# Kernel tuning notes

Hardware: AMD Instinct MI355X
Metric: run time of the kernel (lower is better)

Reference implementation:

```python
import jax, jax.numpy as jnp
import numpy as np

B, H, N, C, E, D, L_OUT, LAYERS = 16, 64, 512, 3, 128, 32, 12, 2


def setup_inputs() -> dict:
    key = jax.random.key(0)
    ks = jax.random.split(key, 16)
    nrm = lambda k, s, sc=1.0: jax.random.normal(k, s, jnp.float32) * sc
    adj = jax.random.uniform(ks[0], (N, N), jnp.float32)
    adj = adj / adj.sum(axis=-1, keepdims=True)  # row-normalized prior adjacency
    return {
        "x_input": nrm(ks[1], (B, H, N, C)),
        "adj": adj,
        "Wf": nrm(ks[2], (3, E, 3 * C), 0.1),
        "Uf": nrm(ks[3], (3, E, E), 0.05),
        "bf": jnp.zeros((3, E), jnp.float32),
        "E1f": nrm(ks[4], (N, D)),
        "E2f": nrm(ks[5], (N, D)),
        "Wb": nrm(ks[6], (3, E, 3 * C), 0.1),
        "Ub": nrm(ks[7], (3, E, E), 0.05),
        "bb": jnp.zeros((3, E), jnp.float32),
        "E1b": nrm(ks[8], (N, D)),
        "E2b": nrm(ks[9], (N, D)),
        "dec_w": nrm(ks[10], (L_OUT, LAYERS, 2 * E), 0.05),  # Conv2d(layer_num->out_len, k=(1,2E)) squeezed
        "dec_b": jnp.zeros((L_OUT,), jnp.float32),
        "out_w": nrm(ks[11], (L_OUT, L_OUT), 0.1),  # 1x1 Conv2d squeezed
        "out_b": jnp.zeros((L_OUT,), jnp.float32),
    }


def _cell_step(c, xt, adj, A_dyn, W, U, b):
    # Graph-coupled GRU cell (IBNCell): xt [B,C,N], c [B,E,N].
    msg = jnp.concatenate(
        [xt,
         jnp.einsum('bcn,nm->bcm', xt, adj),      # prior-graph message passing
         jnp.einsum('bcn,nm->bcm', xt, A_dyn)],   # learned dynamic-graph message passing
        axis=1)  # [B, 3C, N]
    gx = jnp.einsum('goc,bcn->gbon', W, msg)  # 3 stacked gate projections
    r = jax.nn.sigmoid(gx[0] + jnp.einsum('oe,ben->bon', U[0], c) + b[0][:, None])
    u = jax.nn.sigmoid(gx[1] + jnp.einsum('oe,ben->bon', U[1], c) + b[1][:, None])
    g = jnp.tanh(gx[2] + jnp.einsum('oe,ben->bon', U[2], r * c) + b[2][:, None])
    return u * c + (1.0 - u) * g


def _forward(x_input, adj, Wf, Uf, bf, E1f, E2f, Wb, Ub, bb, E1b, E2b, dec_w, dec_b, out_w, out_b):
    # torch: x_input.transpose(-3,-1).transpose(-2,-1) -> [B,C,H,N]; scan layout [H,B,C,N]
    xs = jnp.transpose(x_input, (1, 0, 3, 2))
    A_f = jax.nn.softmax(jax.nn.relu(E1f @ E2f.T), axis=-1)  # dynamic adjacency, fwd cell
    A_b = jax.nn.softmax(jax.nn.relu(E1b @ E2b.T), axis=-1)  # dynamic adjacency, back cell
    c0 = jnp.zeros((xs.shape[1], Wf.shape[1], xs.shape[3]), xs.dtype)  # [B,E,N]

    def step_f(c, xt):
        cn = _cell_step(c, xt, adj, A_f, Wf, Uf, bf)
        return cn, None

    # Output only depends on the last timestep of the bidirectional concat:
    # forward branch -> final state after H steps; backward branch (after flip)
    # at t=H-1 -> its FIRST step (input x[H-1]). Dead per-step outputs elided.
    h_fwd, _ = jax.lax.scan(step_f, c0, xs)
    h_back0 = _cell_step(c0, xs[-1], adj, A_b, Wb, Ub, bb)
    last_ht = jnp.concatenate([h_fwd, h_back0], axis=1)  # [B, 2E, N]

    lt = jnp.transpose(last_ht, (0, 2, 1))  # [B, N, 2E]
    # layer loop z>0 is a no-op on current_layer_output -> final_result repeats last_ht
    final = jnp.broadcast_to(lt[:, None], (lt.shape[0], LAYERS, lt.shape[1], lt.shape[2]))
    h = jnp.einsum('blne,ole->bon', final, dec_w) + dec_b[:, None]  # decoder conv (1,2E)
    return jnp.einsum('oi,bin->bon', out_w, h) + out_b[:, None]  # 1x1 output conv -> [B,L_OUT,N]


def reference(x_input, adj, Wf, Uf, bf, E1f, E2f, Wb, Ub, bb, E1b, E2b, dec_w, dec_b, out_w, out_b):
    return _forward(x_input, adj, Wf, Uf, bf, E1f, E2f, Wb, Ub, bb, E1b, E2b, dec_w, dec_b, out_w, out_b)
```

## Files before the change

kernel.cpp:

```cpp
#include <hip/hip_runtime.h>


typedef _Float16 half8_t __attribute__((ext_vector_type(8)));
typedef float float4_t __attribute__((ext_vector_type(4)));

#define PIN(x) asm volatile("" : "+v"(x))

__device__ __forceinline__ float sigmoidf_(float x) {
  return __builtin_amdgcn_rcpf(1.f + __expf(-x));
}
__device__ __forceinline__ float tanhf_(float x) {
  return fmaf(-2.f, __builtin_amdgcn_rcpf(__expf(2.f * x) + 1.f), 1.f);
}

__global__ __launch_bounds__(256) void prep_kernel(
    const float* __restrict__ E1f, const float* __restrict__ E2f,
    const float* __restrict__ E1b, const float* __restrict__ E2b,
    const float* __restrict__ adj, const float* __restrict__ x,
    const float* __restrict__ Wf, const float* __restrict__ Uf,
    const float* __restrict__ bf, const float* __restrict__ Wb,
    const float* __restrict__ bb, _Float16* __restrict__ adjT,
    _Float16* __restrict__ AfT, _Float16* __restrict__ AbT,
    _Float16* __restrict__ xT16, _Float16* __restrict__ ufrag,
    _Float16* __restrict__ wbfrag) {
  int bid = blockIdx.x;
  int tid = threadIdx.x;
  if (bid >= 1288) {
    int bid2 = bid - 1288;
    int b = bid2 >> 6, t = bid2 & 63;
    const float2* xp = (const float2*)(x + (size_t)(b * 64 + t) * 1536);
    float2 f0 = xp[tid * 3], f1 = xp[tid * 3 + 1], f2 = xp[tid * 3 + 2];
    _Float16* dst = xT16 + (size_t)(b * 64 + t) * 1536;
    int n0_ = tid * 2;
    dst[n0_] = (_Float16)f0.x;
    dst[512 + n0_] = (_Float16)f0.y;
    dst[1024 + n0_] = (_Float16)f1.x;
    dst[n0_ + 1] = (_Float16)f1.y;
    dst[512 + n0_ + 1] = (_Float16)f2.x;
    dst[1024 + n0_ + 1] = (_Float16)f2.y;
    return;
  }
  if (bid >= 1272) {
    int r2 = bid - 1272;
    int gi = 1 + (r2 & 1);
    int og = r2 >> 1;
    for (int e = tid; e < 512; e += 256) {
      int lane = e >> 3, j = e & 7;
      int o = og * 16 + (lane & 15);
      int q = (lane >> 4) * 8 + j;
      float v = (q < 9) ? Wb[gi * 1152 + o * 9 + q]
                        : (q == 9 ? bb[gi * 128 + o] : 0.f);
      wbfrag[r2 * 512 + e] = (_Float16)v;
    }
    return;
  }
  if (bid >= 1152) {
    int r = bid - 1152;
    int kb = r % 5;
    int gi = (r / 5) % 3;
    int og = r / 15;
    for (int e = tid; e < 512; e += 256) {
      int lane = e >> 3, j = e & 7;
      int o = og * 16 + (lane & 15);
      int q4 = lane >> 4;
      float v;
      if (kb < 4) {
        v = Uf[gi * 16384 + o * 128 + kb * 32 + q4 * 8 + j];
      } else {
        int q = q4 * 8 + j;
        v = (q < 9) ? Wf[gi * 1152 + o * 9 + q]
                    : (q == 9 ? bf[gi * 128 + o] : 0.f);
      }
      ufrag[r * 512 + e] = (_Float16)v;
    }
    return;
  }
  if (bid >= 1024) {
    int base = (bid - 1024) * 4;
    for (int r = 0; r < 4; ++r) {
      int row = base + r;
      float v0 = adj[row * 512 + tid];
      float v1 = adj[row * 512 + tid + 256];
      adjT[(size_t)tid * 512 + row] = (_Float16)v0;
      adjT[(size_t)(tid + 256) * 512 + row] = (_Float16)v1;
    }
    return;
  }
  int which = bid >> 9;
  int row = bid & 511;
  const float* E1 = which ? E1b : E1f;
  const float* E2 = which ? E2b : E2f;
  _Float16* A = which ? AbT : AfT;
  __shared__ float e1s[32];
  __shared__ float red[256];
  if (tid < 32) e1s[tid] = E1[row * 32 + tid];
  __syncthreads();
  float s[2];
#pragma unroll
  for (int h = 0; h < 2; ++h) {
    int m = tid + h * 256;
    const float4* e2 = (const float4*)(E2 + m * 32);
    float acc = 0.f;
#pragma unroll
    for (int d4 = 0; d4 < 8; ++d4) {
      float4 v = e2[d4];
      acc = fmaf(v.x, e1s[d4 * 4 + 0], acc);
      acc = fmaf(v.y, e1s[d4 * 4 + 1], acc);
      acc = fmaf(v.z, e1s[d4 * 4 + 2], acc);
      acc = fmaf(v.w, e1s[d4 * 4 + 3], acc);
    }
    s[h] = fmaxf(acc, 0.f);
  }
  red[tid] = fmaxf(s[0], s[1]);
  __syncthreads();
  for (int off = 128; off > 0; off >>= 1) {
    if (tid < off) red[tid] = fmaxf(red[tid], red[tid + off]);
    __syncthreads();
  }
  float mx = red[0];
  __syncthreads();
  float e0 = __expf(s[0] - mx), e1v = __expf(s[1] - mx);
  red[tid] = e0 + e1v;
  __syncthreads();
  for (int off = 128; off > 0; off >>= 1) {
    if (tid < off) red[tid] += red[tid + off];
    __syncthreads();
  }
  float inv = __builtin_amdgcn_rcpf(red[0]);
  A[(size_t)tid * 512 + row] = (_Float16)(e0 * inv);
  A[(size_t)(tid + 256) * 512 + row] = (_Float16)(e1v * inv);
}

__global__ __launch_bounds__(256, 4) void msg_kernel(
    const _Float16* __restrict__ xT16, const _Float16* __restrict__ adjT,
    const _Float16* __restrict__ AfT, const _Float16* __restrict__ AbT,
    _Float16* __restrict__ msg16, _Float16* __restrict__ msgb16) {
  __shared__ __align__(8) _Float16 Sst[512 * 12];
  int tid = threadIdx.x;
  int t = blockIdx.x >> 4;
  int n0g = (blockIdx.x & 15) * 32;
  int lane = tid & 63, og = tid >> 6;
  int l15 = lane & 15, q4 = lane >> 4, q0 = q4 * 8;
  int nt = og & 1, mat = og >> 1;
  bool is63 = (t == 63);
  bool doAb = is63 && (mat == 0);

  const _Float16* Bmat = mat ? AfT : adjT;
  int n = n0g + nt * 16 + l15;

  const float4_t zero4 = {0.f, 0.f, 0.f, 0.f};
  float4_t acc[3], accb[3];
#pragma unroll
  for (int mt = 0; mt < 3; ++mt) { acc[mt] = zero4; accb[mt] = zero4; }

  for (int kb = 0; kb < 16; ++kb) {
    half8_t b0 = *(const half8_t*)&Bmat[(size_t)n * 512 + kb * 32 + q0];
    half8_t b2;
    if (doAb) b2 = *(const half8_t*)&AbT[(size_t)n * 512 + kb * 32 + q0];
#pragma unroll
    for (int mt = 0; mt < 3; ++mt) {
      int m = mt * 16 + l15;
      int bm = (m * 21846) >> 16;
      int cm = m - bm * 3;
      half8_t a = *(const half8_t*)
          &xT16[((size_t)(bm * 64 + t) * 3 + cm) * 512 + kb * 32 + q0];
      acc[mt] = __builtin_amdgcn_mfma_f32_16x16x32_f16(a, b0, acc[mt], 0, 0, 0);
      if (doAb)
        accb[mt] = __builtin_amdgcn_mfma_f32_16x16x32_f16(a, b2, accb[mt], 0, 0, 0);
    }
  }

  for (int i = tid; i < 512; i += 256) {
    int tb = i >> 5, nl = i & 31;
    int nn = n0g + nl;
    _Float16* row = &Sst[i * 12];
#pragma unroll
    for (int c = 0; c < 3; ++c)
      row[c] = xT16[((size_t)(tb * 64 + t) * 3 + c) * 512 + nn];
    row[9] = (_Float16)1.f;
    row[10] = (_Float16)0.f;
    row[11] = (_Float16)0.f;
  }
#pragma unroll
  for (int mt = 0; mt < 3; ++mt)
#pragma unroll
    for (int r = 0; r < 4; ++r) {
      int m = mt * 16 + q4 * 4 + r;
      int tb = (m * 21846) >> 16;
      int c = m - tb * 3;
      Sst[((size_t)tb * 32 + nt * 16 + l15) * 12 + 3 + mat * 3 + c] =
          (_Float16)acc[mt][r];
    }
  __syncthreads();
  for (int i = tid; i < 512; i += 256) {
    int tb = i >> 5, nl = i & 31;
    const uint2* s = (const uint2*)&Sst[i * 12];
    uint2* dst = (uint2*)&msg16[((size_t)(t * 16 + tb) * 512 + n0g + nl) * 12];
    dst[0] = s[0]; dst[1] = s[1]; dst[2] = s[2];
  }
  if (is63) {
    __syncthreads();
    if (mat == 0) {
#pragma unroll
      for (int mt = 0; mt < 3; ++mt)
#pragma unroll
        for (int r = 0; r < 4; ++r) {
          int m = mt * 16 + q4 * 4 + r;
          int tb = (m * 21846) >> 16;
          int c = m - tb * 3;
          Sst[((size_t)tb * 32 + nt * 16 + l15) * 12 + 6 + c] = (_Float16)accb[mt][r];
        }
    }
    __syncthreads();
    for (int i = tid; i < 512; i += 256) {
      int tb = i >> 5, nl = i & 31;
      const uint2* s = (const uint2*)&Sst[i * 12];
      uint2* dst = (uint2*)&msgb16[((size_t)tb * 512 + n0g + nl) * 12];
      dst[0] = s[0]; dst[1] = s[1]; dst[2] = s[2];
    }
  }
}

__global__ __launch_bounds__(512, 4) void rec_kernel(
    const _Float16* __restrict__ msg16, const _Float16* __restrict__ msgb16,
    const _Float16* __restrict__ ufrag, const _Float16* __restrict__ wbfrag,
    const float* __restrict__ dec_w, const float* __restrict__ dec_b,
    const float* __restrict__ out_w, const float* __restrict__ out_b,
    float* __restrict__ out) {
  __shared__ __align__(16) _Float16 Cbuf[4 * 64 * 8];
  __shared__ __align__(16) _Float16 Gbuf[4 * 64 * 8];
  __shared__ float hf_lds[128 * 16];
  __shared__ float hb_lds[128 * 16];
  __shared__ float hdec_lds[12 * 16];
  int tid = threadIdx.x, bid = blockIdx.x;
  int b = bid >> 5;
  int n0 = (bid & 31) * 16;
  int lane = tid & 63, og = tid >> 6;
  int l15 = lane & 15, q4 = lane >> 4;

  half8_t afrag[3][5];
#pragma unroll
  for (int gi = 0; gi < 3; ++gi)
#pragma unroll
    for (int kb = 0; kb < 5; ++kb) {
      afrag[gi][kb] = *(const half8_t*)
          &ufrag[(size_t)(((og * 3 + gi) * 5 + kb) * 512) + lane * 8];
      PIN(afrag[gi][kb]);
    }

  if (tid < 256) {
    uint4 z; z.x = z.y = z.z = z.w = 0;
    ((uint4*)Cbuf)[tid] = z;
  }
  float cr[4] = {0.f, 0.f, 0.f, 0.f};
  __syncthreads();

  const float4_t zero4 = {0.f, 0.f, 0.f, 0.f};
  union H4U { _Float16 h[4]; unsigned long long u; };
  union U16 { uint4 u4; half8_t h8; };
  unsigned odd = q4 & 1;
  const char* mrow = (const char*)msg16 + ((size_t)(b * 512 + n0 + l15)) * 24;
  const size_t tstride = (size_t)16 * 512 * 24;

  U16 bu;
  {
    uint4 lo = *(const uint4*)mrow;
    uint2 hi = *(const uint2*)(mrow + 16);
    bu.u4.x = odd ? hi.x : lo.x;
    bu.u4.y = odd ? hi.y : lo.y;
    bu.u4.z = odd ? 0u : lo.z;
    bu.u4.w = odd ? 0u : lo.w;
  }
  half8_t bm_cur = bu.h8;

  int kb_w = og >> 1;
  int lane_w = ((og & 1) * 2 + (q4 >> 1)) * 16 + l15;
  int j0 = (q4 & 1) * 4;

  for (int t = 0; t < 64; ++t) {
    int tn = (t < 63) ? t + 1 : 63;
    const char* p = mrow + (size_t)tn * tstride;
    uint4 lo = *(const uint4*)p;
    uint2 hi = *(const uint2*)(p + 16);

    half8_t cf[4];
#pragma unroll
    for (int kb = 0; kb < 4; ++kb)
      cf[kb] = *(const half8_t*)&Cbuf[(kb * 64 + lane) * 8];

    float4_t accr = zero4, accu = zero4;
#pragma unroll
    for (int kb = 0; kb < 4; ++kb) {
      accr = __builtin_amdgcn_mfma_f32_16x16x32_f16(afrag[0][kb], cf[kb], accr, 0, 0, 0);
      accu = __builtin_amdgcn_mfma_f32_16x16x32_f16(afrag[1][kb], cf[kb], accu, 0, 0, 0);
    }
    accr = __builtin_amdgcn_mfma_f32_16x16x32_f16(afrag[0][4], bm_cur, accr, 0, 0, 0);
    accu = __builtin_amdgcn_mfma_f32_16x16x32_f16(afrag[1][4], bm_cur, accu, 0, 0, 0);
    float4_t accg = __builtin_amdgcn_mfma_f32_16x16x32_f16(afrag[2][4], bm_cur, zero4, 0, 0, 0);

    {
      H4U v;
#pragma unroll
      for (int r = 0; r < 4; ++r)
        v.h[r] = (_Float16)(sigmoidf_(accr[r]) * cr[r]);
      *(unsigned long long*)&Gbuf[(kb_w * 64 + lane_w) * 8 + j0] = v.u;
    }
    __syncthreads();

    half8_t gf[4];
#pragma unroll
    for (int kb = 0; kb < 4; ++kb)
      gf[kb] = *(const half8_t*)&Gbuf[(kb * 64 + lane) * 8];
#pragma unroll
    for (int kb = 0; kb < 4; ++kb)
      accg = __builtin_amdgcn_mfma_f32_16x16x32_f16(afrag[2][kb], gf[kb], accg, 0, 0, 0);

    {
      H4U v;
#pragma unroll
      for (int r = 0; r < 4; ++r) {
        float uu = sigmoidf_(accu[r]);
        float gg = tanhf_(accg[r]);
        float cn = fmaf(uu, cr[r] - gg, gg);
        cr[r] = cn;
        v.h[r] = (_Float16)cn;
      }
      *(unsigned long long*)&Cbuf[(kb_w * 64 + lane_w) * 8 + j0] = v.u;
    }
    __syncthreads();

    bu.u4.x = odd ? hi.x : lo.x;
    bu.u4.y = odd ? hi.y : lo.y;
    bu.u4.z = odd ? 0u : lo.z;
    bu.u4.w = odd ? 0u : lo.w;
    bm_cur = bu.h8;
  }

  {
    const char* p = (const char*)msgb16 + ((size_t)(b * 512 + n0 + l15)) * 24;
    uint4 lo = *(const uint4*)p;
    uint2 hi = *(const uint2*)(p + 16);
    U16 bb2;
    bb2.u4.x = odd ? hi.x : lo.x;
    bb2.u4.y = odd ? hi.y : lo.y;
    bb2.u4.z = odd ? 0u : lo.z;
    bb2.u4.w = odd ? 0u : lo.w;
    half8_t au_f = *(const half8_t*)&wbfrag[(size_t)((og * 2 + 0) * 512) + lane * 8];
    half8_t ag_f = *(const half8_t*)&wbfrag[(size_t)((og * 2 + 1) * 512) + lane * 8];
    float4_t au = __builtin_amdgcn_mfma_f32_16x16x32_f16(au_f, bb2.h8, zero4, 0, 0, 0);
    float4_t ag = __builtin_amdgcn_mfma_f32_16x16x32_f16(ag_f, bb2.h8, zero4, 0, 0, 0);
#pragma unroll
    for (int r = 0; r < 4; ++r) {
      int row = og * 16 + q4 * 4 + r;
      float uu = sigmoidf_(au[r]);
      float gg = tanhf_(ag[r]);
      hb_lds[row * 16 + l15] = (1.f - uu) * gg;
      hf_lds[row * 16 + l15] = cr[r];
    }
  }
  __syncthreads();

  if (tid < 192) {
    int i = tid >> 4, cc = tid & 15;
    const float* dwa = dec_w + (size_t)i * 512;
    const float* dwb = dwa + 256;
    float hd = dec_b[i];
    for (int e = 0; e < 128; ++e) {
      hd = fmaf(dwa[e] + dwb[e], hf_lds[e * 16 + cc], hd);
      hd = fmaf(dwa[128 + e] + dwb[128 + e], hb_lds[e * 16 + cc], hd);
    }
    hdec_lds[i * 16 + cc] = hd;
  }
  __syncthreads();
  if (tid < 192) {
    int o = tid >> 4, cc = tid & 15;
    float v = out_b[o];
#pragma unroll
    for (int i = 0; i < 12; ++i) v = fmaf(out_w[o * 12 + i], hdec_lds[i * 16 + cc], v);
    out[((size_t)(b * 12 + o)) * 512 + n0 + cc] = v;
  }
}

extern "C" void kernel_launch(void* const* d_in, const int* in_sizes, int n_in,
                              void* d_out, int out_size, void* d_ws, size_t ws_size,
                              hipStream_t stream) {
  (void)in_sizes; (void)n_in; (void)out_size; (void)ws_size;
  const float* x     = (const float*)d_in[0];
  const float* adj   = (const float*)d_in[1];
  const float* Wf    = (const float*)d_in[2];
  const float* Uf    = (const float*)d_in[3];
  const float* bf    = (const float*)d_in[4];
  const float* E1f   = (const float*)d_in[5];
  const float* E2f   = (const float*)d_in[6];
  const float* Wb    = (const float*)d_in[7];
  const float* bb    = (const float*)d_in[9];
  const float* E1b   = (const float*)d_in[10];
  const float* E2b   = (const float*)d_in[11];
  const float* dec_w = (const float*)d_in[12];
  const float* dec_b = (const float*)d_in[13];
  const float* out_w = (const float*)d_in[14];
  const float* out_b = (const float*)d_in[15];

  _Float16* h      = (_Float16*)d_ws;
  _Float16* adjT   = h;
  _Float16* AfT    = h + 262144;
  _Float16* AbT    = h + 524288;
  _Float16* xT16   = h + 786432;
  _Float16* ufrag  = h + 2359296;
  _Float16* wbfrag = h + 2420736;
  _Float16* msg16  = h + 2428928;
  _Float16* msgb16 = h + 8720384;

  prep_kernel<<<2312, 256, 0, stream>>>(E1f, E2f, E1b, E2b, adj, x, Wf, Uf, bf,
                                        Wb, bb, adjT, AfT, AbT, xT16, ufrag, wbfrag);
  msg_kernel<<<1024, 256, 0, stream>>>(xT16, adjT, AfT, AbT, msg16, msgb16);
  rec_kernel<<<512, 512, 0, stream>>>(msg16, msgb16, ufrag, wbfrag,
                                      dec_w, dec_b, out_w, out_b, (float*)d_out);
}
```

Measured before the change: 220.0 us.

## Fold exp2 scaling into gate weights and tile-transpose adjacency matrices

Gate weight fragments are pre-scaled by -log2(e) or 2*log2(e) so the recurrent loop's sigmoid and tanh become a raw exp2 plus a reciprocal, with no per-element multiply. Half conversion now uses packed round-toward-zero converts. The strided transposed writes of adj and the softmax matrices in prep are replaced by row-major writes plus a separate LDS-tiled transpose kernel, aiming for coalesced global stores. This costs an extra kernel launch and a second pass over the softmax matrices, and the fp16 rounding of the scaled weights changes slightly.

```diff
diff --git a/kernel.cpp b/kernel.cpp
--- a/kernel.cpp
+++ b/kernel.cpp
@@ -2,31 +2,27 @@
 
 
 typedef _Float16 half8_t __attribute__((ext_vector_type(8)));
+typedef __fp16 fp16x2_t __attribute__((ext_vector_type(2)));
 typedef float float4_t __attribute__((ext_vector_type(4)));
 
 #define PIN(x) asm volatile("" : "+v"(x))
 
-__device__ __forceinline__ float sigmoidf_(float x) {
-  return __builtin_amdgcn_rcpf(1.f + __expf(-x));
-}
-__device__ __forceinline__ float tanhf_(float x) {
-  return fmaf(-2.f, __builtin_amdgcn_rcpf(__expf(2.f * x) + 1.f), 1.f);
-}
+__device__ __forceinline__ float exp2_(float x) { return __builtin_amdgcn_exp2f(x); }
+__device__ __forceinline__ float rcp_(float x) { return __builtin_amdgcn_rcpf(x); }
 
 __global__ __launch_bounds__(256) void prep_kernel(
     const float* __restrict__ E1f, const float* __restrict__ E2f,
     const float* __restrict__ E1b, const float* __restrict__ E2b,
-    const float* __restrict__ adj, const float* __restrict__ x,
-    const float* __restrict__ Wf, const float* __restrict__ Uf,
-    const float* __restrict__ bf, const float* __restrict__ Wb,
-    const float* __restrict__ bb, _Float16* __restrict__ adjT,
-    _Float16* __restrict__ AfT, _Float16* __restrict__ AbT,
+    const float* __restrict__ x, const float* __restrict__ Wf,
+    const float* __restrict__ Uf, const float* __restrict__ bf,
+    const float* __restrict__ Wb, const float* __restrict__ bb,
+    _Float16* __restrict__ AfR, _Float16* __restrict__ AbR,
     _Float16* __restrict__ xT16, _Float16* __restrict__ ufrag,
     _Float16* __restrict__ wbfrag) {
   int bid = blockIdx.x;
   int tid = threadIdx.x;
-  if (bid >= 1288) {
-    int bid2 = bid - 1288;
+  if (bid >= 1160) {
+    int bid2 = bid - 1160;
     int b = bid2 >> 6, t = bid2 & 63;
     const float2* xp = (const float2*)(x + (size_t)(b * 64 + t) * 1536);
     float2 f0 = xp[tid * 3], f1 = xp[tid * 3 + 1], f2 = xp[tid * 3 + 2];
@@ -40,25 +36,27 @@
     dst[1024 + n0_ + 1] = (_Float16)f2.y;
     return;
   }
-  if (bid >= 1272) {
-    int r2 = bid - 1272;
+  if (bid >= 1144) {
+    int r2 = bid - 1144;
     int gi = 1 + (r2 & 1);
     int og = r2 >> 1;
+    float scl = (gi == 2) ? 2.8853902f : -1.4426950f;
     for (int e = tid; e < 512; e += 256) {
       int lane = e >> 3, j = e & 7;
       int o = og * 16 + (lane & 15);
       int q = (lane >> 4) * 8 + j;
       float v = (q < 9) ? Wb[gi * 1152 + o * 9 + q]
                         : (q == 9 ? bb[gi * 128 + o] : 0.f);
-      wbfrag[r2 * 512 + e] = (_Float16)v;
+      wbfrag[r2 * 512 + e] = (_Float16)(v * scl);
     }
     return;
   }
-  if (bid >= 1152) {
-    int r = bid - 1152;
+  if (bid >= 1024) {
+    int r = bid - 1024;
     int kb = r % 5;
     int gi = (r / 5) % 3;
     int og = r / 15;
+    float scl = (gi == 2) ? 2.8853902f : -1.4426950f;
     for (int e = tid; e < 512; e += 256) {
       int lane = e >> 3, j = e & 7;
       int o = og * 16 + (lane & 15);
@@ -71,18 +69,7 @@
         v = (q < 9) ? Wf[gi * 1152 + o * 9 + q]
                     : (q == 9 ? bf[gi * 128 + o] : 0.f);
       }
-      ufrag[r * 512 + e] = (_Float16)v;
-    }
-    return;
-  }
-  if (bid >= 1024) {
-    int base = (bid - 1024) * 4;
-    for (int r = 0; r < 4; ++r) {
-      int row = base + r;
-      float v0 = adj[row * 512 + tid];
-      float v1 = adj[row * 512 + tid + 256];
-      adjT[(size_t)tid * 512 + row] = (_Float16)v0;
-      adjT[(size_t)(tid + 256) * 512 + row] = (_Float16)v1;
+      ufrag[r * 512 + e] = (_Float16)(v * scl);
     }
     return;
   }
@@ -90,7 +77,7 @@
   int row = bid & 511;
   const float* E1 = which ? E1b : E1f;
   const float* E2 = which ? E2b : E2f;
-  _Float16* A = which ? AbT : AfT;
+  _Float16* A = which ? AbR : AfR;
   __shared__ float e1s[32];
   __shared__ float red[256];
   if (tid < 32) e1s[tid] = E1[row * 32 + tid];
@@ -126,9 +113,37 @@
     if (tid < off) red[tid] += red[tid + off];
     __syncthreads();
   }
-  float inv = __builtin_amdgcn_rcpf(red[0]);
-  A[(size_t)tid * 512 + row] = (_Float16)(e0 * inv);
-  A[(size_t)(tid + 256) * 512 + row] = (_Float16)(e1v * inv);
+  float inv = rcp_(red[0]);
+  A[(size_t)row * 512 + tid] = (_Float16)(e0 * inv);
+  A[(size_t)row * 512 + tid + 256] = (_Float16)(e1v * inv);
+}
+
+__global__ __launch_bounds__(256) void transpose_kernel(
+    const float* __restrict__ adj, const _Float16* __restrict__ AfR,
+    const _Float16* __restrict__ AbR, _Float16* __restrict__ adjT,
+    _Float16* __restrict__ AfT, _Float16* __restrict__ AbT) {
+  __shared__ _Float16 T[64][65];
+  int bid = blockIdx.x;
+  int mat = bid >> 6;
+  int tile = bid & 63;
+  int tr = tile >> 3, tc = tile & 7;
+  int t = threadIdx.x;
+  int r = t >> 2, cb = (t & 3) * 16;
+  if (mat == 0) {
+    const float* s = adj + (size_t)(tr * 64 + r) * 512 + tc * 64 + cb;
+#pragma unroll
+    for (int i = 0; i < 16; ++i) T[r][cb + i] = (_Float16)s[i];
+  } else {
+    const _Float16* s =
+        (mat == 1 ? AfR : AbR) + (size_t)(tr * 64 + r) * 512 + tc * 64 + cb;
+#pragma unroll
+    for (int i = 0; i < 16; ++i) T[r][cb + i] = s[i];
+  }
+  __syncthreads();
+  _Float16* d = (mat == 0 ? adjT : mat == 1 ? AfT : AbT) +
+                (size_t)(tc * 64 + r) * 512 + tr * 64 + cb;
+#pragma unroll
+  for (int i = 0; i < 16; ++i) d[i] = T[cb + i][r];
 }
 
 __global__ __launch_bounds__(256, 4) void msg_kernel(
@@ -227,14 +242,15 @@
     const float* __restrict__ dec_w, const float* __restrict__ dec_b,
     const float* __restrict__ out_w, const float* __restrict__ out_b,
     float* __restrict__ out) {
-  __shared__ __align__(16) _Float16 Cbuf[4 * 64 * 8];
-  __shared__ __align__(16) _Float16 Gbuf[4 * 64 * 8];
+  __shared__ __align__(16) _Float16 Cbuf[2048];
+  __shared__ __align__(16) _Float16 Gbuf[2048];
   __shared__ float hf_lds[128 * 16];
   __shared__ float hb_lds[128 * 16];
   __shared__ float hdec_lds[12 * 16];
   int tid = threadIdx.x, bid = blockIdx.x;
   int b = bid >> 5;
-  int n0 = (bid & 31) * 16;
+  int nt = bid & 31;
+  int n0 = nt * 16;
   int lane = tid & 63, og = tid >> 6;
   int l15 = lane & 15, q4 = lane >> 4;
 
@@ -253,14 +269,13 @@
     ((uint4*)Cbuf)[tid] = z;
   }
   float cr[4] = {0.f, 0.f, 0.f, 0.f};
-  __syncthreads();
 
   const float4_t zero4 = {0.f, 0.f, 0.f, 0.f};
-  union H4U { _Float16 h[4]; unsigned long long u; };
+  union H4U { fp16x2_t h2[2]; unsigned long long u; };
   union U16 { uint4 u4; half8_t h8; };
   unsigned odd = q4 & 1;
+  const size_t tstride = (size_t)16 * 512 * 24;
   const char* mrow = (const char*)msg16 + ((size_t)(b * 512 + n0 + l15)) * 24;
-  const size_t tstride = (size_t)16 * 512 * 24;
 
   U16 bu;
   {
@@ -271,11 +286,12 @@
     bu.u4.z = odd ? 0u : lo.z;
     bu.u4.w = odd ? 0u : lo.w;
   }
-  half8_t bm_cur = bu.h8;
+  half8_t bm = bu.h8;
 
   int kb_w = og >> 1;
   int lane_w = ((og & 1) * 2 + (q4 >> 1)) * 16 + l15;
   int j0 = (q4 & 1) * 4;
+  __syncthreads();
 
   for (int t = 0; t < 64; ++t) {
     int tn = (t < 63) ? t + 1 : 63;
@@ -294,37 +310,42 @@
       accr = __builtin_amdgcn_mfma_f32_16x16x32_f16(afrag[0][kb], cf[kb], accr, 0, 0, 0);
       accu = __builtin_amdgcn_mfma_f32_16x16x32_f16(afrag[1][kb], cf[kb], accu, 0, 0, 0);
     }
-    accr = __builtin_amdgcn_mfma_f32_16x16x32_f16(afrag[0][4], bm_cur, accr, 0, 0, 0);
-    accu = __builtin_amdgcn_mfma_f32_16x16x32_f16(afrag[1][4], bm_cur, accu, 0, 0, 0);
-    float4_t accg = __builtin_amdgcn_mfma_f32_16x16x32_f16(afrag[2][4], bm_cur, zero4, 0, 0, 0);
+    accr = __builtin_amdgcn_mfma_f32_16x16x32_f16(afrag[0][4], bm, accr, 0, 0, 0);
+    accu = __builtin_amdgcn_mfma_f32_16x16x32_f16(afrag[1][4], bm, accu, 0, 0, 0);
+    float4_t accg = __builtin_amdgcn_mfma_f32_16x16x32_f16(afrag[2][4], bm, zero4, 0, 0, 0);
+
+    {
+      float rc0 = rcp_(1.f + exp2_(accr[0])) * cr[0];
+      float rc1 = rcp_(1.f + exp2_(accr[1])) * cr[1];
+      float rc2 = rcp_(1.f + exp2_(accr[2])) * cr[2];
+      float rc3 = rcp_(1.f + exp2_(accr[3])) * cr[3];
+      H4U v;
+      v.h2[0] = __builtin_amdgcn_cvt_pkrtz(rc0, rc1);
+      v.h2[1] = __builtin_amdgcn_cvt_pkrtz(rc2, rc3);
+      *(unsigned long long*)&Gbuf[(kb_w * 64 + lane_w) * 8 + j0] = v.u;
+    }
+    __syncthreads();
+
+    half8_t gf[4];
+#pragma unroll
+    for (int kb = 0; kb < 4; ++kb)
+      gf[kb] = *(const half8_t*)&Gbuf[(kb * 64 + lane) * 8];
+#pragma unroll
+    for (int kb = 0; kb < 4; ++kb)
+      accg = __builtin_amdgcn_mfma_f32_16x16x32_f16(afrag[2][kb], gf[kb], accg, 0, 0, 0);
 
     {
       H4U v;
-#pragma unroll
-      for (int r = 0; r < 4; ++r)
-        v.h[r] = (_Float16)(sigmoidf_(accr[r]) * cr[r]);
-      *(unsigned long long*)&Gbuf[(kb_w * 64 + lane_w) * 8 + j0] = v.u;
-    }
-    __syncthreads();
-
-    half8_t gf[4];
-#pragma unroll
-    for (int kb = 0; kb < 4; ++kb)
-      gf[kb] = *(const half8_t*)&Gbuf[(kb * 64 + lane) * 8];
-#pragma unroll
-    for (int kb = 0; kb < 4; ++kb)
-      accg = __builtin_amdgcn_mfma_f32_16x16x32_f16(afrag[2][kb], gf[kb], accg, 0, 0, 0);
-
-    {
-      H4U v;
+      float cn[4];
 #pragma unroll
       for (int r = 0; r < 4; ++r) {
-        float uu = sigmoidf_(accu[r]);
-        float gg = tanhf_(accg[r]);
-        float cn = fmaf(uu, cr[r] - gg, gg);
-        cr[r] = cn;
-        v.h[r] = (_Float16)cn;
+        float uu = rcp_(1.f + exp2_(accu[r]));
+        float gg = fmaf(-2.f, rcp_(exp2_(accg[r]) + 1.f), 1.f);
+        cn[r] = fmaf(uu, cr[r] - gg, gg);
+        cr[r] = cn[r];
       }
+      v.h2[0] = __builtin_amdgcn_cvt_pkrtz(cn[0], cn[1]);
+      v.h2[1] = __builtin_amdgcn_cvt_pkrtz(cn[2], cn[3]);
       *(unsigned long long*)&Cbuf[(kb_w * 64 + lane_w) * 8 + j0] = v.u;
     }
     __syncthreads();
@@ -333,7 +354,7 @@
     bu.u4.y = odd ? hi.y : lo.y;
     bu.u4.z = odd ? 0u : lo.z;
     bu.u4.w = odd ? 0u : lo.w;
-    bm_cur = bu.h8;
+    bm = bu.h8;
   }
 
   {
@@ -352,8 +373,8 @@
 #pragma unroll
     for (int r = 0; r < 4; ++r) {
       int row = og * 16 + q4 * 4 + r;
-      float uu = sigmoidf_(au[r]);
-      float gg = tanhf_(ag[r]);
+      float uu = rcp_(1.f + exp2_(au[r]));
+      float gg = fmaf(-2.f, rcp_(exp2_(ag[r]) + 1.f), 1.f);
       hb_lds[row * 16 + l15] = (1.f - uu) * gg;
       hf_lds[row * 16 + l15] = cr[r];
     }
@@ -405,14 +426,17 @@
   _Float16* adjT   = h;
   _Float16* AfT    = h + 262144;
   _Float16* AbT    = h + 524288;
-  _Float16* xT16   = h + 786432;
-  _Float16* ufrag  = h + 2359296;
-  _Float16* wbfrag = h + 2420736;
+  _Float16* ufrag  = h + 786432;
+  _Float16* wbfrag = h + 847872;
+  _Float16* xT16   = h + 856064;
   _Float16* msg16  = h + 2428928;
   _Float16* msgb16 = h + 8720384;
-
-  prep_kernel<<<2312, 256, 0, stream>>>(E1f, E2f, E1b, E2b, adj, x, Wf, Uf, bf,
-                                        Wb, bb, adjT, AfT, AbT, xT16, ufrag, wbfrag);
+  _Float16* AfR    = h + 8818688;
+  _Float16* AbR    = h + 9080832;
+
+  prep_kernel<<<2184, 256, 0, stream>>>(E1f, E2f, E1b, E2b, x, Wf, Uf, bf,
+                                        Wb, bb, AfR, AbR, xT16, ufrag, wbfrag);
+  transpose_kernel<<<192, 256, 0, stream>>>(adj, AfR, AbR, adjT, AfT, AbT);
   msg_kernel<<<1024, 256, 0, stream>>>(xT16, adjT, AfT, AbT, msg16, msgb16);
   rec_kernel<<<512, 512, 0, stream>>>(msg16, msgb16, ufrag, wbfrag,
                                       dec_w, dec_b, out_w, out_b, (float*)d_out);
```

Result: no change. 216.4 us (-1.6%).
